# Performance work log

Measured on AMD Instinct MI355X. Metric: run time of the kernel, lower is better.

Reference implementation:

```python
import jax, jax.numpy as jnp
import numpy as np

IMG = 160      # img_size
P = 100        # img_pathch_num = (160/16)^2
NBLK = 256     # pixels per 16x16 patch
NCLS = 4

def _index_matrix():
    # faithful port of NewAIFV.index_init
    ind = np.arange(256)
    start = (ind // 16) * IMG + (ind % 16) * 16
    idx = np.zeros(NBLK * P, dtype=np.int32)
    for i in range(P):
        idx[i * 256:(i + 1) * 256] = start + (i // 16) * 16 * IMG + (i % 16)
    return jnp.asarray(idx)

_IDX = _index_matrix()


def setup_inputs() -> dict:
    key = jax.random.key(0)
    ks = jax.random.split(key, 7)
    B, C = 4, 256
    return {
        "feat_S": jax.random.normal(ks[0], (B, C, IMG, IMG), jnp.float32),
        "feat_T": jax.random.normal(ks[1], (B, C, IMG, IMG), jnp.float32),
        "Pred_S": jax.random.normal(ks[2], (B, NCLS, IMG, IMG), jnp.float32),
        "Pred_T": jax.random.normal(ks[3], (B, NCLS, IMG, IMG), jnp.float32),
        "S_atten": jax.random.normal(ks[4], (B, P, P), jnp.float32),
        "T_atten": jax.random.normal(ks[5], (B, P, P), jnp.float32),
        "target": jax.random.randint(ks[6], (B, 1, IMG, IMG), 0, NCLS, jnp.int32),
    }


def _cos(a, b):
    # torch.nn.CosineSimilarity(dim=1): dot / max(|a||b|, 1e-8)
    num = (a * b).sum(1)
    den = jnp.maximum(jnp.sqrt((a * a).sum(1)) * jnp.sqrt((b * b).sum(1)), 1e-8)
    return num / den


def reference(feat_S, feat_T, Pred_S, Pred_T, S_atten, T_atten, target):
    B, C, H, W = feat_S.shape
    hw = H * W
    idx = _IDX
    # gathered patch reorder (index_select along flattened spatial dim)
    fS = feat_S.reshape(B, C, hw)[:, :, idx]
    fT = feat_T.reshape(B, C, hw)[:, :, idx]
    tg = target.reshape(B, 1, hw)[:, :, idx].reshape(B, 1, H, W)
    # 256-iteration loop of per-patch [B,C,100]@[B,100,100] matmuls -> one einsum
    TS = jnp.einsum('bcik,bkj->bcij', fS.reshape(B, C, NBLK, P), S_atten).reshape(B, C, H, W)
    TT = jnp.einsum('bcik,bkj->bcij', fT.reshape(B, C, NBLK, P), T_atten).reshape(B, C, H, W)
    ScS = jax.nn.softmax(Pred_S, axis=1).reshape(B, NCLS, hw)[:, :, idx].reshape(B, NCLS, H, W)
    ScT = jax.nn.softmax(Pred_T, axis=1).reshape(B, NCLS, hw)[:, :, idx].reshape(B, NCLS, H, W)
    dt = TS.dtype
    one_hot = (tg == jnp.arange(NCLS)[None, :, None, None]).astype(dt)   # [B,4,H,W]
    wei_s = (ScS * one_hot).sum(1)  # [B,H,W]
    wei_t = (ScT * one_hot).sum(1)
    tf = tg.astype(dt)  # [B,1,H,W], broadcast replaces nn.Upsample+expand

    def centers(class_list, s_prto, t_prto, eps):
        cS, cT = TS, TT
        for i in range(NCLS):
            j = class_list[i]
            stmp = ScT[:, j:j + 1]              # [B,1,H,W] (Score_Tmp, broadcast over C)
            m = (tf == i).astype(dt)            # mask_feat (class i)
            mp = (tf == j).astype(dt)           # mask_feat_prto (class class_list[i])
            denS = (mp if s_prto else m).sum((-1, -2)) + eps          # [B,1]
            protoS = ((mp * TS).sum((-1, -2)) / denS)[:, :, None, None]
            denT = (stmp * (mp if t_prto else m)).sum((-1, -2)) + eps
            protoT = ((mp * TT * stmp).sum((-1, -2)) / denT)[:, :, None, None]
            cS = (1 - m) * cS + m * protoS
            cT = (1 - m) * cT + m * protoT
        return cS, cT

    # three variants exactly as in the torch loops (denominator choices differ)
    cS0, cT0 = centers([1, 0, 3, 2], False, False, 1e-6)
    cS1, cT1 = centers([2, 3, 0, 1], True, True, 1e-6)
    cS2, cT2 = centers([3, 2, 1, 0], True, True, 1.0)

    w = (1 - wei_s) * wei_t
    vec_s = jnp.stack([w * _cos(TS, c) for c in (cS0, cS1, cS2)], axis=1)  # [B,3,H,W]
    vec_t = jnp.stack([w * _cos(TT, c) for c in (cT0, cT1, cT2)], axis=1)
    return jnp.mean((vec_s - vec_t) ** 2)
```

## Files before the change

kernel.cpp:

```cpp
#include <hip/hip_runtime.h>
#include <cstdint>
#include <cstddef>

#define HW 25600

typedef __attribute__((ext_vector_type(8))) short bf16x8;
typedef __attribute__((ext_vector_type(16))) float f32x16;

union ABu { bf16x8 v; uint2 u[2]; };

__device__ __forceinline__ f32x16 zero16() {
    f32x16 z;
#pragma unroll
    for (int i = 0; i < 16; ++i) z[i] = 0.f;
    return z;
}

__device__ __forceinline__ unsigned short f2bf(float x) {
    unsigned u = __builtin_bit_cast(unsigned, x);
    unsigned r = (u + 0x7FFF + ((u >> 16) & 1)) >> 16;
    return (unsigned short)r;
}

__device__ __forceinline__ float bf2f(unsigned short s) {
    return __builtin_bit_cast(float, (unsigned)s << 16);
}

__device__ __forceinline__ float wred(float v) {
#pragma unroll
    for (int off = 32; off; off >>= 1) v += __shfl_down(v, off, 64);
    return v;
}

__device__ double blockReduce256D(double v, double* s4) {
#pragma unroll
    for (int off = 32; off; off >>= 1) v += __shfl_down(v, off, 64);
    __syncthreads();
    if ((threadIdx.x & 63) == 0) s4[threadIdx.x >> 6] = v;
    __syncthreads();
    return s4[0] + s4[1] + s4[2] + s4[3];
}

__global__ __launch_bounds__(256) void k1_prep(
    const float* __restrict__ PredS, const float* __restrict__ PredT,
    const int* __restrict__ target,
    int* __restrict__ cls_arr, float* __restrict__ wT_arr,
    float* __restrict__ w_arr, float* __restrict__ partial_prep)
{
    __shared__ float sL[4][20];
    int blk = blockIdx.x;
    int b = blk / 100, r = blk - b * 100;
    int t = threadIdx.x, w = t >> 6, lane = t & 63;
    int ql = r * 256 + t;
    int v = ((t >> 4) * 160) + ((t & 15) * 16) + ((r >> 4) * 2560) + (r & 15);

    int cls = target[b * HW + v];

    const float* pS = PredS + b * 4 * HW + v;
    float a0 = pS[0], a1 = pS[HW], a2 = pS[2 * HW], a3 = pS[3 * HW];
    float mS = fmaxf(fmaxf(a0, a1), fmaxf(a2, a3));
    float e0 = expf(a0 - mS), e1 = expf(a1 - mS), e2 = expf(a2 - mS), e3 = expf(a3 - mS);
    float invS = 1.0f / (e0 + e1 + e2 + e3);
    float wei_s = ((cls == 0) ? e0 : (cls == 1) ? e1 : (cls == 2) ? e2 : e3) * invS;

    const float* pT = PredT + b * 4 * HW + v;
    float c0 = pT[0], c1 = pT[HW], c2 = pT[2 * HW], c3 = pT[3 * HW];
    float mT = fmaxf(fmaxf(c0, c1), fmaxf(c2, c3));
    float f0 = expf(c0 - mT), f1 = expf(c1 - mT), f2 = expf(c2 - mT), f3 = expf(c3 - mT);
    float invT = 1.0f / (f0 + f1 + f2 + f3);
    float tn0 = f0 * invT, tn1 = f1 * invT, tn2 = f2 * invT, tn3 = f3 * invT;
    float wei_t = (cls == 0) ? tn0 : (cls == 1) ? tn1 : (cls == 2) ? tn2 : tn3;

    cls_arr[b * HW + ql] = cls;
    wT_arr[b * HW + ql] = wei_t;
    w_arr[b * HW + ql] = (1.0f - wei_s) * wei_t;

    float vals[20];
#pragma unroll
    for (int s = 0; s < 4; ++s) vals[s] = (cls == s) ? 1.f : 0.f;
#pragma unroll
    for (int i2 = 0; i2 < 4; ++i2) {
        vals[4 + i2 * 4 + 0] = (cls == i2) ? tn0 : 0.f;
        vals[4 + i2 * 4 + 1] = (cls == i2) ? tn1 : 0.f;
        vals[4 + i2 * 4 + 2] = (cls == i2) ? tn2 : 0.f;
        vals[4 + i2 * 4 + 3] = (cls == i2) ? tn3 : 0.f;
    }
#pragma unroll
    for (int s = 0; s < 20; ++s) {
        float rv = wred(vals[s]);
        if (lane == 0) sL[w][s] = rv;
    }
    __syncthreads();
    if (t < 20) {
        int ob = blk * 20;
        partial_prep[ob + t] = sL[0][t] + sL[1][t] + sL[2][t] + sL[3][t];
    }
}

__global__ void k15_red(const float* __restrict__ partial_prep,
                        float* __restrict__ cnt, float* __restrict__ E)
{
    int t = threadIdx.x;
    if (t < 80) {
        int b = t / 20, s = t - (t / 20) * 20;
        float a = 0.f;
        for (int r = 0; r < 100; ++r) a += partial_prep[(b * 100 + r) * 20 + s];
        if (s < 4) cnt[b * 4 + s] = a;
        else       E[b * 16 + (s - 4)] = a;
    }
}

__global__ __launch_bounds__(128) void k2_w(
    const float* __restrict__ Satt, const float* __restrict__ Tatt,
    const int* __restrict__ cls_arr, const float* __restrict__ wT_arr,
    unsigned short* __restrict__ Wbf_S, unsigned short* __restrict__ Wbf_T)
{
    __shared__ float Al[100 * 101];
    __shared__ int cls_s[100];
    __shared__ float wTs[100];
    int blk = blockIdx.x;
    int b = blk >> 8, i = blk & 255;
    int t = threadIdx.x;
    if (t < 100) {
        cls_s[t] = cls_arr[b * HW + i * 100 + t];
        wTs[t] = wT_arr[b * HW + i * 100 + t];
    }
    for (int f = t; f < 10000; f += 128) Al[f + f / 100] = Satt[b * 10000 + f];
    __syncthreads();
    if (t < 100) {
        float a0 = 0, a1 = 0, a2 = 0, a3 = 0;
        for (int jc = 0; jc < 100; ++jc) {
            float a = Al[t * 101 + jc];
            int cc = cls_s[jc];
            a0 += (cc == 0) ? a : 0.f;
            a1 += (cc == 1) ? a : 0.f;
            a2 += (cc == 2) ? a : 0.f;
            a3 += (cc == 3) ? a : 0.f;
        }
        uint2 pk;
        pk.x = (unsigned)f2bf(a0) | ((unsigned)f2bf(a1) << 16);
        pk.y = (unsigned)f2bf(a2) | ((unsigned)f2bf(a3) << 16);
        *(uint2*)(Wbf_S + (size_t)(b * HW + i * 100 + t) * 4) = pk;
    }
    __syncthreads();
    for (int f = t; f < 10000; f += 128) Al[f + f / 100] = Tatt[b * 10000 + f];
    __syncthreads();
    if (t < 100) {
        float a0 = 0, a1 = 0, a2 = 0, a3 = 0;
        for (int jc = 0; jc < 100; ++jc) {
            float a = Al[t * 101 + jc] * wTs[jc];
            int cc = cls_s[jc];
            a0 += (cc == 0) ? a : 0.f;
            a1 += (cc == 1) ? a : 0.f;
            a2 += (cc == 2) ? a : 0.f;
            a3 += (cc == 3) ? a : 0.f;
        }
        uint2 pk;
        pk.x = (unsigned)f2bf(a0) | ((unsigned)f2bf(a1) << 16);
        pk.y = (unsigned)f2bf(a2) | ((unsigned)f2bf(a3) << 16);
        *(uint2*)(Wbf_T + (size_t)(b * HW + i * 100 + t) * 4) = pk;
    }
}

__global__ __launch_bounds__(256) void k3_scan(
    const float* __restrict__ feat, const unsigned short* __restrict__ Wbf,
    unsigned short* __restrict__ featP, float* __restrict__ pp)
{
    __shared__ unsigned short ldsW[16 * 260 + 8];
    __shared__ float sL[16];
    int x = blockIdx.x;
    int c = x & 255;
    int bd = x >> 8;
    int D = bd % 7, b = bd / 7;
    int t = threadIdx.x, w = t >> 6, lane = t & 63;

    const float* fbase = feat + (size_t)(b * 256 + c) * HW + 2560 * D;
#pragma unroll
    for (int ra = 0; ra < 4; ++ra) {
        int A = (t >> 6) + 4 * ra;
        int f4i = t & 63;
        float4 fx = *(const float4*)(fbase + 160 * A + 4 * f4i);
        uint2 pk;
        pk.x = (unsigned)f2bf(fx.x) | ((unsigned)f2bf(fx.y) << 16);
        pk.y = (unsigned)f2bf(fx.z) | ((unsigned)f2bf(fx.w) << 16);
        *(uint2*)(ldsW + A * 260 + 4 * f4i) = pk;
    }
    __syncthreads();

    float as0 = 0.f, as1 = 0.f, as2 = 0.f, as3 = 0.f;
    int nr = (D < 6) ? 2 : 1;
    for (int rep = 0; rep < nr; ++rep) {
        if (D == 6 && t >= 128) break;
        int pl = rep * 2048 + t * 8;
        int Pb = D * 4096 + pl;
        int4 w4[4];
        {
            const int4* wp = (const int4*)(Wbf + ((size_t)b * HW + Pb) * 4);
            w4[0] = wp[0]; w4[1] = wp[1]; w4[2] = wp[2]; w4[3] = wp[3];
        }
        int A = (t & 31) >> 1;
        int base_unit = A * 260 + 128 * (t & 1) + rep * 8 + (t >> 5);
        unsigned short us[8];
        float fv[8];
#pragma unroll
        for (int e = 0; e < 8; ++e) {
            us[e] = ldsW[base_unit + 16 * e];
            fv[e] = bf2f(us[e]);
        }
        const unsigned short* ww = (const unsigned short*)w4;
#pragma unroll
        for (int e = 0; e < 8; ++e) {
            as0 += fv[e] * bf2f(ww[e * 4 + 0]);
            as1 += fv[e] * bf2f(ww[e * 4 + 1]);
            as2 += fv[e] * bf2f(ww[e * 4 + 2]);
            as3 += fv[e] * bf2f(ww[e * 4 + 3]);
        }
        int4 outp;
        ((unsigned*)&outp)[0] = (unsigned)us[0] | ((unsigned)us[1] << 16);
        ((unsigned*)&outp)[1] = (unsigned)us[2] | ((unsigned)us[3] << 16);
        ((unsigned*)&outp)[2] = (unsigned)us[4] | ((unsigned)us[5] << 16);
        ((unsigned*)&outp)[3] = (unsigned)us[6] | ((unsigned)us[7] << 16);
        *(int4*)(featP + (size_t)(b * 256 + c) * HW + Pb) = outp;
    }

    float rv0 = wred(as0), rv1 = wred(as1), rv2 = wred(as2), rv3 = wred(as3);
    if (lane == 0) {
        sL[w * 4 + 0] = rv0; sL[w * 4 + 1] = rv1;
        sL[w * 4 + 2] = rv2; sL[w * 4 + 3] = rv3;
    }
    __syncthreads();
    if (t < 4) {
        pp[x * 4 + t] = sL[t] + sL[4 + t] + sL[8 + t] + sL[12 + t];
    }
}

__global__ void k35_red(const float* __restrict__ pp, float* __restrict__ Sum)
{
    int id = blockIdx.x * 256 + threadIdx.x;
    if (id < 4096) {
        int bc = id >> 2, j = id & 3;
        int b = bc >> 8, c = bc & 255;
        float a = 0.f;
        for (int D = 0; D < 7; ++D)
            a += pp[(((b * 7 + D) * 256) + c) * 4 + j];
        Sum[id] = a;
    }
}

__global__ __launch_bounds__(256, 2) void k4_mfma(
    const unsigned short* __restrict__ featP,
    const float* __restrict__ Att,
    const float* __restrict__ Sum,
    float* __restrict__ n2h, float* __restrict__ doth)
{
    __shared__ __align__(16) unsigned short featL[32 * 408 + 16];
    __shared__ __align__(16) unsigned short attL[100 * 136];

    int x = blockIdx.x;
    int chalf = x & 1, b = (x >> 1) & 3, g = x >> 3;
    int t = threadIdx.x, w = t >> 6, l = t & 63;

    for (int f = t; f < 13600; f += 256) attL[f] = 0;
    featL[(t >> 3) * 408 + 400 + (t & 7)] = 0;
    if (t < 16) featL[32 * 408 + t] = 0;
    __syncthreads();
    for (int f = t; f < 10000; f += 256) {
        int k = f / 100, j = f - k * 100;
        attL[j * 136 + k] = f2bf(Att[b * 10000 + f]);
    }

    float n2a[4] = {0, 0, 0, 0};
    float dota[4][4] = {};

    int lj = l & 31, lh = l >> 5;
    const unsigned short* brow0 = attL + (0 * 32 + lj) * 136 + lh * 8;
    const unsigned short* brow1 = attL + (1 * 32 + lj) * 136 + lh * 8;
    const unsigned short* brow2 = attL + (2 * 32 + lj) * 136 + lh * 8;
    int j3 = 96 + lj; if (j3 > 99) j3 = 99;
    const unsigned short* brow3 = attL + j3 * 136 + lh * 8;
    const unsigned short* arow = featL + lj * 408 + w * 100 + lh * 8;

#pragma unroll 1
    for (int ch = 0; ch < 4; ++ch) {
        __syncthreads();
        {
            const unsigned short* src = featP + (size_t)(b * 256 + chalf * 128 + ch * 32 + (t >> 3)) * HW
                                        + g * 400 + (t & 7) * 8;
            unsigned short* dst = featL + (t >> 3) * 408 + (t & 7) * 8;
#pragma unroll
            for (int i = 0; i < 7; ++i) {
                int cb = (t & 7) + i * 8;
                if (cb < 50)
                    *(int4*)(dst + i * 64) = *(const int4*)(src + i * 64);
            }
        }
        __syncthreads();

        f32x16 acc0 = zero16(), acc1 = zero16(), acc2 = zero16(), acc3 = zero16();
#pragma unroll
        for (int ks = 0; ks < 7; ++ks) {
            ABu aF;
            aF.u[0] = *(const uint2*)(arow + ks * 16);
            aF.u[1] = *(const uint2*)(arow + ks * 16 + 4);
            bf16x8 b0 = *(const bf16x8*)(brow0 + ks * 16);
            acc0 = __builtin_amdgcn_mfma_f32_32x32x16_bf16(aF.v, b0, acc0, 0, 0, 0);
            bf16x8 b1 = *(const bf16x8*)(brow1 + ks * 16);
            acc1 = __builtin_amdgcn_mfma_f32_32x32x16_bf16(aF.v, b1, acc1, 0, 0, 0);
            bf16x8 b2 = *(const bf16x8*)(brow2 + ks * 16);
            acc2 = __builtin_amdgcn_mfma_f32_32x32x16_bf16(aF.v, b2, acc2, 0, 0, 0);
            bf16x8 b3 = *(const bf16x8*)(brow3 + ks * 16);
            acc3 = __builtin_amdgcn_mfma_f32_32x32x16_bf16(aF.v, b3, acc3, 0, 0, 0);
        }

        int cb0 = chalf * 128 + ch * 32 + (lh << 2);
#pragma unroll
        for (int r = 0; r < 16; ++r) {
            int cl = (r & 3) + ((r >> 2) << 3);
            float4 sv = *(const float4*)(Sum + (size_t)(b * 256 + cb0 + cl) * 4);
            float v;
            v = acc0[r]; n2a[0] += v * v;
            dota[0][0] += v * sv.x; dota[0][1] += v * sv.y; dota[0][2] += v * sv.z; dota[0][3] += v * sv.w;
            v = acc1[r]; n2a[1] += v * v;
            dota[1][0] += v * sv.x; dota[1][1] += v * sv.y; dota[1][2] += v * sv.z; dota[1][3] += v * sv.w;
            v = acc2[r]; n2a[2] += v * v;
            dota[2][0] += v * sv.x; dota[2][1] += v * sv.y; dota[2][2] += v * sv.z; dota[2][3] += v * sv.w;
            v = acc3[r]; n2a[3] += v * v;
            dota[3][0] += v * sv.x; dota[3][1] += v * sv.y; dota[3][2] += v * sv.z; dota[3][3] += v * sv.w;
        }
    }

#pragma unroll
    for (int nt = 0; nt < 4; ++nt) {
        n2a[nt] += __shfl_down(n2a[nt], 32, 64);
#pragma unroll
        for (int m = 0; m < 4; ++m) dota[nt][m] += __shfl_down(dota[nt][m], 32, 64);
    }
    if (l < 32) {
        int i0 = g * 4 + w;
        int pqb = b * HW + i0 * 100;
#pragma unroll
        for (int nt = 0; nt < 4; ++nt) {
            int j = nt * 32 + l;
            if (j < 100) {
                n2h[chalf * 102400 + pqb + j] = n2a[nt];
                float4 dv = {dota[nt][0], dota[nt][1], dota[nt][2], dota[nt][3]};
                *(float4*)(doth + chalf * 409600 + (size_t)(pqb + j) * 4) = dv;
            }
        }
    }
}

__global__ void k45_tbl(const float* __restrict__ SumTS, const float* __restrict__ SumTT,
                        const float* __restrict__ cnt, const float* __restrict__ E,
                        float* __restrict__ tbl)
{
    int t = threadIdx.x;
    if (t < 32) {
        int b = t >> 3, sj = t & 7, stv = sj >> 2, j = sj & 3;
        const float* S = stv ? SumTT : SumTS;
        float s = 0.f;
        for (int c = 0; c < 256; ++c) {
            float x = S[(b * 256 + c) * 4 + j];
            s += x * x;
        }
        tbl[b * 32 + stv * 4 + j] = sqrtf(s);
    } else if (t < 48) {
        int q = t - 32;
        int b = q >> 2, i = q & 3;
        tbl[b * 32 + 8 + 0 * 4 + i] = cnt[b * 4 + i] + 1e-6f;
        tbl[b * 32 + 8 + 1 * 4 + i] = cnt[b * 4 + (i ^ 2)] + 1e-6f;
        tbl[b * 32 + 8 + 2 * 4 + i] = cnt[b * 4 + (i ^ 3)] + 1.0f;
        tbl[b * 32 + 20 + 0 * 4 + i] = E[b * 16 + i * 4 + (i ^ 1)] + 1e-6f;
        tbl[b * 32 + 20 + 1 * 4 + i] = E[b * 16 + 5 * (i ^ 2)] + 1e-6f;
        tbl[b * 32 + 20 + 2 * 4 + i] = E[b * 16 + 5 * (i ^ 3)] + 1.0f;
    }
}

__global__ __launch_bounds__(256) void k5_final(
    const int* __restrict__ cls_arr, const float* __restrict__ w_arr,
    const float* __restrict__ n2S, const float* __restrict__ n2T,
    const float* __restrict__ dotS, const float* __restrict__ dotT,
    const float* __restrict__ tbl, double* __restrict__ partial_res)
{
    __shared__ double s4[4];
    int blk = blockIdx.x;
    int b = blk / 100, r = blk - b * 100;
    int t = threadIdx.x;
    int pq = b * HW + r * 256 + t;

    int i = cls_arr[pq];
    float wv = w_arr[pq];
    float sqS = sqrtf(n2S[pq] + n2S[102400 + pq]);
    float sqT = sqrtf(n2T[pq] + n2T[102400 + pq]);
    float4 dSa = *(const float4*)(dotS + (size_t)pq * 4);
    float4 dSb = *(const float4*)(dotS + 409600 + (size_t)pq * 4);
    float4 dTa = *(const float4*)(dotT + (size_t)pq * 4);
    float4 dTb = *(const float4*)(dotT + 409600 + (size_t)pq * 4);
    float4 dS = {dSa.x + dSb.x, dSa.y + dSb.y, dSa.z + dSb.z, dSa.w + dSb.w};
    float4 dT = {dTa.x + dTb.x, dTa.y + dTb.y, dTa.z + dTb.z, dTa.w + dTb.w};
    const float* tb = tbl + b * 32;

    double acc = 0.0;
#pragma unroll
    for (int v = 0; v < 3; ++v) {
        int j = i ^ (v + 1);
        float dsj = (j == 0) ? dS.x : (j == 1) ? dS.y : (j == 2) ? dS.z : dS.w;
        float dtj = (j == 0) ? dT.x : (j == 1) ? dT.y : (j == 2) ? dT.z : dT.w;
        float cnS = tb[j], cnT = tb[4 + j];
        float denS = tb[8 + v * 4 + i], denT = tb[20 + v * 4 + i];
        float cs = (dsj / denS) / fmaxf(sqS * (cnS / denS), 1e-8f);
        float ct = (dtj / denT) / fmaxf(sqT * (cnT / denT), 1e-8f);
        float vs = wv * cs, vt = wv * ct;
        float d = vs - vt;
        acc += (double)d * (double)d;
    }
    double tot = blockReduce256D(acc, s4);
    if (t == 0) partial_res[blk] = tot;
}

__global__ void k6_out(const double* __restrict__ partial_res, float* __restrict__ out)
{
    if (threadIdx.x == 0 && blockIdx.x == 0) {
        double s = 0.0;
        for (int q = 0; q < 400; ++q) s += partial_res[q];
        out[0] = (float)(s / 307200.0);
    }
}

extern "C" void kernel_launch(void* const* d_in, const int* in_sizes, int n_in,
                              void* d_out, int out_size, void* d_ws, size_t ws_size,
                              hipStream_t stream)
{
    const float* feat_S  = (const float*)d_in[0];
    const float* feat_T  = (const float*)d_in[1];
    const float* Pred_S  = (const float*)d_in[2];
    const float* Pred_T  = (const float*)d_in[3];
    const float* S_atten = (const float*)d_in[4];
    const float* T_atten = (const float*)d_in[5];
    const int*   target  = (const int*)d_in[6];

    float* ws = (float*)d_ws;
    unsigned short* featP = (unsigned short*)d_ws;
    unsigned short* WbfS  = (unsigned short*)(ws + 13107200);
    unsigned short* WbfT  = (unsigned short*)(ws + 13312000);
    int*   cls_a = (int*)(ws + 13516800);
    float* wT_a  = ws + 13619200;
    float* w_a   = ws + 13721600;
    float* SumTS = ws + 13824000;
    float* SumTT = ws + 13828096;
    float* n2S   = ws + 13832192;
    float* n2T   = ws + 14036992;
    float* dotS  = ws + 14241792;
    float* dotT  = ws + 15060992;
    float* pprep = ws + 15880192;
    float* cnt   = ws + 15888192;
    float* E     = ws + 15888208;
    float* tbl   = ws + 15888272;
    double* pres = (double*)(ws + 15888400);
    float* ppart = ws + 15889200;

    k1_prep<<<400, 256, 0, stream>>>(Pred_S, Pred_T, target, cls_a, wT_a, w_a, pprep);
    k15_red<<<1, 128, 0, stream>>>(pprep, cnt, E);
    k2_w<<<1024, 128, 0, stream>>>(S_atten, T_atten, cls_a, wT_a, WbfS, WbfT);

    k3_scan<<<7168, 256, 0, stream>>>(feat_S, WbfS, featP, ppart);
    k35_red<<<16, 256, 0, stream>>>(ppart, SumTS);
    k4_mfma<<<512, 256, 0, stream>>>(featP, S_atten, SumTS, n2S, dotS);
    k3_scan<<<7168, 256, 0, stream>>>(feat_T, WbfT, featP, ppart);
    k35_red<<<16, 256, 0, stream>>>(ppart, SumTT);
    k4_mfma<<<512, 256, 0, stream>>>(featP, T_atten, SumTT, n2T, dotT);

    k45_tbl<<<1, 64, 0, stream>>>(SumTS, SumTT, cnt, E, tbl);
    k5_final<<<400, 256, 0, stream>>>(cls_a, w_a, n2S, n2T, dotS, dotT, tbl, pres);
    k6_out<<<1, 64, 0, stream>>>(pres, (float*)d_out);
}
```

Baseline: 173.2 us.

## Merge S/T passes into single launches and parallelize small reductions

Processes the student and teacher sides in the same k3_scan and k4_mfma launches by doubling the grid and giving each side its own featP buffer. k3_scan now handles four channels per block and reuses the attention weights kept in registers across them. k4_mfma preloads the B operand into registers instead of reading it from LDS on every step. The k15 reduction is folded into k2_w as extra blocks, and k45_tbl and k6_out become wave and block reductions rather than serial loops. This cuts the launch count and exposes more parallelism, at the cost of a workspace twice as large and more register pressure in k4.

```diff
diff --git a/kernel.cpp b/kernel.cpp
--- a/kernel.cpp
+++ b/kernel.cpp
@@ -8,6 +8,7 @@
 typedef __attribute__((ext_vector_type(16))) float f32x16;
 
 union ABu { bf16x8 v; uint2 u[2]; };
+union B128 { bf16x8 v; int4 q; };
 
 __device__ __forceinline__ f32x16 zero16() {
     f32x16 z;
@@ -97,30 +98,29 @@
     }
 }
 
-__global__ void k15_red(const float* __restrict__ partial_prep,
-                        float* __restrict__ cnt, float* __restrict__ E)
-{
-    int t = threadIdx.x;
-    if (t < 80) {
-        int b = t / 20, s = t - (t / 20) * 20;
-        float a = 0.f;
-        for (int r = 0; r < 100; ++r) a += partial_prep[(b * 100 + r) * 20 + s];
-        if (s < 4) cnt[b * 4 + s] = a;
-        else       E[b * 16 + (s - 4)] = a;
-    }
-}
-
 __global__ __launch_bounds__(128) void k2_w(
     const float* __restrict__ Satt, const float* __restrict__ Tatt,
     const int* __restrict__ cls_arr, const float* __restrict__ wT_arr,
-    unsigned short* __restrict__ Wbf_S, unsigned short* __restrict__ Wbf_T)
-{
+    unsigned short* __restrict__ Wbf_S, unsigned short* __restrict__ Wbf_T,
+    const float* __restrict__ partial_prep, float* __restrict__ cnt, float* __restrict__ E)
+{
+    int blk = blockIdx.x;
+    int t = threadIdx.x;
+    if (blk >= 1024) {
+        int i = blk - 1024;
+        if (t < 64) {
+            int b = i / 20, s = i - (i / 20) * 20;
+            float a = partial_prep[(b * 100 + t) * 20 + s];
+            if (t + 64 < 100) a += partial_prep[(b * 100 + t + 64) * 20 + s];
+            a = wred(a);
+            if (t == 0) { if (s < 4) cnt[b * 4 + s] = a; else E[b * 16 + (s - 4)] = a; }
+        }
+        return;
+    }
     __shared__ float Al[100 * 101];
     __shared__ int cls_s[100];
     __shared__ float wTs[100];
-    int blk = blockIdx.x;
     int b = blk >> 8, i = blk & 255;
-    int t = threadIdx.x;
     if (t < 100) {
         cls_s[t] = cls_arr[b * HW + i * 100 + t];
         wTs[t] = wT_arr[b * HW + i * 100 + t];
@@ -163,102 +163,129 @@
 }
 
 __global__ __launch_bounds__(256) void k3_scan(
-    const float* __restrict__ feat, const unsigned short* __restrict__ Wbf,
+    const float* __restrict__ featS, const float* __restrict__ featT,
+    const unsigned short* __restrict__ WbfS, const unsigned short* __restrict__ WbfT,
     unsigned short* __restrict__ featP, float* __restrict__ pp)
 {
     __shared__ unsigned short ldsW[16 * 260 + 8];
     __shared__ float sL[16];
     int x = blockIdx.x;
-    int c = x & 255;
-    int bd = x >> 8;
+    int side = x & 1;
+    int rest = x >> 1;
+    int cq = rest & 63;
+    int bd = rest >> 6;
     int D = bd % 7, b = bd / 7;
     int t = threadIdx.x, w = t >> 6, lane = t & 63;
 
-    const float* fbase = feat + (size_t)(b * 256 + c) * HW + 2560 * D;
-#pragma unroll
-    for (int ra = 0; ra < 4; ++ra) {
-        int A = (t >> 6) + 4 * ra;
-        int f4i = t & 63;
-        float4 fx = *(const float4*)(fbase + 160 * A + 4 * f4i);
-        uint2 pk;
-        pk.x = (unsigned)f2bf(fx.x) | ((unsigned)f2bf(fx.y) << 16);
-        pk.y = (unsigned)f2bf(fx.z) | ((unsigned)f2bf(fx.w) << 16);
-        *(uint2*)(ldsW + A * 260 + 4 * f4i) = pk;
-    }
-    __syncthreads();
-
-    float as0 = 0.f, as1 = 0.f, as2 = 0.f, as3 = 0.f;
+    const float* feat = side ? featT : featS;
+    const unsigned short* Wbf = side ? WbfT : WbfS;
+    unsigned short* fP = featP + (size_t)side * 26214400u;
+    int ppbase = side * 28672 + ((b * 7 + D) * 256) * 4;
+
     int nr = (D < 6) ? 2 : 1;
-    for (int rep = 0; rep < nr; ++rep) {
-        if (D == 6 && t >= 128) break;
-        int pl = rep * 2048 + t * 8;
-        int Pb = D * 4096 + pl;
-        int4 w4[4];
-        {
+    bool act = !(D == 6 && t >= 128);
+
+    int4 w4[2][4];
+#pragma unroll
+    for (int rep = 0; rep < 2; ++rep) {
+        if (rep < nr && act) {
+            int Pb = D * 4096 + rep * 2048 + t * 8;
             const int4* wp = (const int4*)(Wbf + ((size_t)b * HW + Pb) * 4);
-            w4[0] = wp[0]; w4[1] = wp[1]; w4[2] = wp[2]; w4[3] = wp[3];
-        }
-        int A = (t & 31) >> 1;
-        int base_unit = A * 260 + 128 * (t & 1) + rep * 8 + (t >> 5);
-        unsigned short us[8];
-        float fv[8];
-#pragma unroll
-        for (int e = 0; e < 8; ++e) {
-            us[e] = ldsW[base_unit + 16 * e];
-            fv[e] = bf2f(us[e]);
-        }
-        const unsigned short* ww = (const unsigned short*)w4;
-#pragma unroll
-        for (int e = 0; e < 8; ++e) {
-            as0 += fv[e] * bf2f(ww[e * 4 + 0]);
-            as1 += fv[e] * bf2f(ww[e * 4 + 1]);
-            as2 += fv[e] * bf2f(ww[e * 4 + 2]);
-            as3 += fv[e] * bf2f(ww[e * 4 + 3]);
-        }
-        int4 outp;
-        ((unsigned*)&outp)[0] = (unsigned)us[0] | ((unsigned)us[1] << 16);
-        ((unsigned*)&outp)[1] = (unsigned)us[2] | ((unsigned)us[3] << 16);
-        ((unsigned*)&outp)[2] = (unsigned)us[4] | ((unsigned)us[5] << 16);
-        ((unsigned*)&outp)[3] = (unsigned)us[6] | ((unsigned)us[7] << 16);
-        *(int4*)(featP + (size_t)(b * 256 + c) * HW + Pb) = outp;
-    }
-
-    float rv0 = wred(as0), rv1 = wred(as1), rv2 = wred(as2), rv3 = wred(as3);
-    if (lane == 0) {
-        sL[w * 4 + 0] = rv0; sL[w * 4 + 1] = rv1;
-        sL[w * 4 + 2] = rv2; sL[w * 4 + 3] = rv3;
-    }
-    __syncthreads();
-    if (t < 4) {
-        pp[x * 4 + t] = sL[t] + sL[4 + t] + sL[8 + t] + sL[12 + t];
-    }
-}
-
-__global__ void k35_red(const float* __restrict__ pp, float* __restrict__ Sum)
+            w4[rep][0] = wp[0]; w4[rep][1] = wp[1]; w4[rep][2] = wp[2]; w4[rep][3] = wp[3];
+        }
+    }
+
+    for (int cv = 0; cv < 4; ++cv) {
+        int c = cq * 4 + cv;
+        const float* fbase = feat + (size_t)(b * 256 + c) * HW + 2560 * D;
+#pragma unroll
+        for (int ra = 0; ra < 4; ++ra) {
+            int A = (t >> 6) + 4 * ra;
+            int f4i = t & 63;
+            float4 fx = *(const float4*)(fbase + 160 * A + 4 * f4i);
+            uint2 pk;
+            pk.x = (unsigned)f2bf(fx.x) | ((unsigned)f2bf(fx.y) << 16);
+            pk.y = (unsigned)f2bf(fx.z) | ((unsigned)f2bf(fx.w) << 16);
+            *(uint2*)(ldsW + A * 260 + 4 * f4i) = pk;
+        }
+        __syncthreads();
+
+        float as0 = 0.f, as1 = 0.f, as2 = 0.f, as3 = 0.f;
+        if (act) {
+#pragma unroll
+            for (int rep = 0; rep < 2; ++rep) {
+                if (rep < nr) {
+                    int Pb = D * 4096 + rep * 2048 + t * 8;
+                    int A2 = (t & 31) >> 1;
+                    int base_unit = A2 * 260 + 128 * (t & 1) + rep * 8 + (t >> 5);
+                    unsigned short us[8];
+                    float fv[8];
+#pragma unroll
+                    for (int e = 0; e < 8; ++e) {
+                        us[e] = ldsW[base_unit + 16 * e];
+                        fv[e] = bf2f(us[e]);
+                    }
+                    const unsigned short* ww = (const unsigned short*)w4[rep];
+#pragma unroll
+                    for (int e = 0; e < 8; ++e) {
+                        as0 += fv[e] * bf2f(ww[e * 4 + 0]);
+                        as1 += fv[e] * bf2f(ww[e * 4 + 1]);
+                        as2 += fv[e] * bf2f(ww[e * 4 + 2]);
+                        as3 += fv[e] * bf2f(ww[e * 4 + 3]);
+                    }
+                    int4 outp;
+                    ((unsigned*)&outp)[0] = (unsigned)us[0] | ((unsigned)us[1] << 16);
+                    ((unsigned*)&outp)[1] = (unsigned)us[2] | ((unsigned)us[3] << 16);
+                    ((unsigned*)&outp)[2] = (unsigned)us[4] | ((unsigned)us[5] << 16);
+                    ((unsigned*)&outp)[3] = (unsigned)us[6] | ((unsigned)us[7] << 16);
+                    *(int4*)(fP + (size_t)(b * 256 + c) * HW + Pb) = outp;
+                }
+            }
+        }
+
+        float rv0 = wred(as0), rv1 = wred(as1), rv2 = wred(as2), rv3 = wred(as3);
+        if (lane == 0) {
+            sL[w * 4 + 0] = rv0; sL[w * 4 + 1] = rv1;
+            sL[w * 4 + 2] = rv2; sL[w * 4 + 3] = rv3;
+        }
+        __syncthreads();
+        if (t < 4) pp[ppbase + c * 4 + t] = sL[t] + sL[4 + t] + sL[8 + t] + sL[12 + t];
+        __syncthreads();
+    }
+}
+
+__global__ void k35_red(const float* __restrict__ pp, float* __restrict__ SumAll)
 {
     int id = blockIdx.x * 256 + threadIdx.x;
-    if (id < 4096) {
-        int bc = id >> 2, j = id & 3;
-        int b = bc >> 8, c = bc & 255;
-        float a = 0.f;
-        for (int D = 0; D < 7; ++D)
-            a += pp[(((b * 7 + D) * 256) + c) * 4 + j];
-        Sum[id] = a;
-    }
+    int side = id >> 12;
+    int rem = id & 4095;
+    int bc = rem >> 2, j = rem & 3;
+    int b = bc >> 8, c = bc & 255;
+    float a = 0.f;
+    for (int D = 0; D < 7; ++D)
+        a += pp[side * 28672 + (((b * 7 + D) * 256) + c) * 4 + j];
+    SumAll[side * 4096 + bc * 4 + j] = a;
 }
 
 __global__ __launch_bounds__(256, 2) void k4_mfma(
     const unsigned short* __restrict__ featP,
-    const float* __restrict__ Att,
-    const float* __restrict__ Sum,
-    float* __restrict__ n2h, float* __restrict__ doth)
+    const float* __restrict__ SattG, const float* __restrict__ TattG,
+    const float* __restrict__ SumAll,
+    float* __restrict__ n2S, float* __restrict__ n2T,
+    float* __restrict__ dotS, float* __restrict__ dotT)
 {
     __shared__ __align__(16) unsigned short featL[32 * 408 + 16];
     __shared__ __align__(16) unsigned short attL[100 * 136];
 
     int x = blockIdx.x;
-    int chalf = x & 1, b = (x >> 1) & 3, g = x >> 3;
+    int side = x & 1, chalf = (x >> 1) & 1, b = (x >> 2) & 3, g = x >> 4;
     int t = threadIdx.x, w = t >> 6, l = t & 63;
+
+    const float* Att = side ? TattG : SattG;
+    const float* Sum = SumAll + side * 4096;
+    const unsigned short* fP = featP + (size_t)side * 26214400u;
+    float* n2h = side ? n2T : n2S;
+    float* doth = side ? dotT : dotS;
 
     for (int f = t; f < 13600; f += 256) attL[f] = 0;
     featL[(t >> 3) * 408 + 400 + (t & 7)] = 0;
@@ -268,23 +295,29 @@
         int k = f / 100, j = f - k * 100;
         attL[j * 136 + k] = f2bf(Att[b * 10000 + f]);
     }
+    __syncthreads();
+
+    int lj = l & 31, lh = l >> 5;
+    bf16x8 breg[7][4];
+    {
+        int j3 = 96 + lj; if (j3 > 99) j3 = 99;
+        int rowoff[4] = { lj, 32 + lj, 64 + lj, j3 };
+#pragma unroll
+        for (int ks = 0; ks < 7; ++ks)
+#pragma unroll
+            for (int s = 0; s < 4; ++s)
+                breg[ks][s] = ((const B128*)(attL + rowoff[s] * 136 + lh * 8 + ks * 16))->v;
+    }
 
     float n2a[4] = {0, 0, 0, 0};
     float dota[4][4] = {};
-
-    int lj = l & 31, lh = l >> 5;
-    const unsigned short* brow0 = attL + (0 * 32 + lj) * 136 + lh * 8;
-    const unsigned short* brow1 = attL + (1 * 32 + lj) * 136 + lh * 8;
-    const unsigned short* brow2 = attL + (2 * 32 + lj) * 136 + lh * 8;
-    int j3 = 96 + lj; if (j3 > 99) j3 = 99;
-    const unsigned short* brow3 = attL + j3 * 136 + lh * 8;
     const unsigned short* arow = featL + lj * 408 + w * 100 + lh * 8;
 
 #pragma unroll 1
     for (int ch = 0; ch < 4; ++ch) {
         __syncthreads();
         {
-            const unsigned short* src = featP + (size_t)(b * 256 + chalf * 128 + ch * 32 + (t >> 3)) * HW
+            const unsigned short* src = fP + (size_t)(b * 256 + chalf * 128 + ch * 32 + (t >> 3)) * HW
                                         + g * 400 + (t & 7) * 8;
             unsigned short* dst = featL + (t >> 3) * 408 + (t & 7) * 8;
 #pragma unroll
@@ -302,14 +335,10 @@
             ABu aF;
             aF.u[0] = *(const uint2*)(arow + ks * 16);
             aF.u[1] = *(const uint2*)(arow + ks * 16 + 4);
-            bf16x8 b0 = *(const bf16x8*)(brow0 + ks * 16);
-            acc0 = __builtin_amdgcn_mfma_f32_32x32x16_bf16(aF.v, b0, acc0, 0, 0, 0);
-            bf16x8 b1 = *(const bf16x8*)(brow1 + ks * 16);
-            acc1 = __builtin_amdgcn_mfma_f32_32x32x16_bf16(aF.v, b1, acc1, 0, 0, 0);
-            bf16x8 b2 = *(const bf16x8*)(brow2 + ks * 16);
-            acc2 = __builtin_amdgcn_mfma_f32_32x32x16_bf16(aF.v, b2, acc2, 0, 0, 0);
-            bf16x8 b3 = *(const bf16x8*)(brow3 + ks * 16);
-            acc3 = __builtin_amdgcn_mfma_f32_32x32x16_bf16(aF.v, b3, acc3, 0, 0, 0);
+            acc0 = __builtin_amdgcn_mfma_f32_32x32x16_bf16(aF.v, breg[ks][0], acc0, 0, 0, 0);
+            acc1 = __builtin_amdgcn_mfma_f32_32x32x16_bf16(aF.v, breg[ks][1], acc1, 0, 0, 0);
+            acc2 = __builtin_amdgcn_mfma_f32_32x32x16_bf16(aF.v, breg[ks][2], acc2, 0, 0, 0);
+            acc3 = __builtin_amdgcn_mfma_f32_32x32x16_bf16(aF.v, breg[ks][3], acc3, 0, 0, 0);
         }
 
         int cb0 = chalf * 128 + ch * 32 + (lh << 2);
@@ -354,19 +383,20 @@
                         const float* __restrict__ cnt, const float* __restrict__ E,
                         float* __restrict__ tbl)
 {
-    int t = threadIdx.x;
-    if (t < 32) {
-        int b = t >> 3, sj = t & 7, stv = sj >> 2, j = sj & 3;
+    int blk = blockIdx.x, t = threadIdx.x;
+    if (blk < 32) {
+        int b = blk >> 3, sj = blk & 7, stv = sj >> 2, j = sj & 3;
         const float* S = stv ? SumTT : SumTS;
         float s = 0.f;
-        for (int c = 0; c < 256; ++c) {
-            float x = S[(b * 256 + c) * 4 + j];
-            s += x * x;
-        }
-        tbl[b * 32 + stv * 4 + j] = sqrtf(s);
-    } else if (t < 48) {
-        int q = t - 32;
-        int b = q >> 2, i = q & 3;
+#pragma unroll
+        for (int u = 0; u < 4; ++u) {
+            float xx = S[(b * 256 + t * 4 + u) * 4 + j];
+            s += xx * xx;
+        }
+        s = wred(s);
+        if (t == 0) tbl[b * 32 + stv * 4 + j] = sqrtf(s);
+    } else if (t < 16) {
+        int b = t >> 2, i = t & 3;
         tbl[b * 32 + 8 + 0 * 4 + i] = cnt[b * 4 + i] + 1e-6f;
         tbl[b * 32 + 8 + 1 * 4 + i] = cnt[b * 4 + (i ^ 2)] + 1e-6f;
         tbl[b * 32 + 8 + 2 * 4 + i] = cnt[b * 4 + (i ^ 3)] + 1.0f;
@@ -418,13 +448,14 @@
     if (t == 0) partial_res[blk] = tot;
 }
 
-__global__ void k6_out(const double* __restrict__ partial_res, float* __restrict__ out)
-{
-    if (threadIdx.x == 0 && blockIdx.x == 0) {
-        double s = 0.0;
-        for (int q = 0; q < 400; ++q) s += partial_res[q];
-        out[0] = (float)(s / 307200.0);
-    }
+__global__ __launch_bounds__(256) void k6_out(const double* __restrict__ partial_res,
+                                              float* __restrict__ out)
+{
+    __shared__ double s4[4];
+    int t = threadIdx.x;
+    double v = (t < 200) ? (partial_res[t] + partial_res[t + 200]) : 0.0;
+    double tot = blockReduce256D(v, s4);
+    if (t == 0) out[0] = (float)(tot / 307200.0);
 }
 
 extern "C" void kernel_launch(void* const* d_in, const int* in_sizes, int n_in,
@@ -441,36 +472,30 @@
 
     float* ws = (float*)d_ws;
     unsigned short* featP = (unsigned short*)d_ws;
-    unsigned short* WbfS  = (unsigned short*)(ws + 13107200);
-    unsigned short* WbfT  = (unsigned short*)(ws + 13312000);
-    int*   cls_a = (int*)(ws + 13516800);
-    float* wT_a  = ws + 13619200;
-    float* w_a   = ws + 13721600;
-    float* SumTS = ws + 13824000;
-    float* SumTT = ws + 13828096;
-    float* n2S   = ws + 13832192;
-    float* n2T   = ws + 14036992;
-    float* dotS  = ws + 14241792;
-    float* dotT  = ws + 15060992;
-    float* pprep = ws + 15880192;
-    float* cnt   = ws + 15888192;
-    float* E     = ws + 15888208;
-    float* tbl   = ws + 15888272;
-    double* pres = (double*)(ws + 15888400);
-    float* ppart = ws + 15889200;
+    unsigned short* WbfS  = (unsigned short*)(ws + 26214400);
+    unsigned short* WbfT  = (unsigned short*)(ws + 26419200);
+    int*   cls_a = (int*)(ws + 26624000);
+    float* wT_a  = ws + 26726400;
+    float* w_a   = ws + 26828800;
+    float* SumTS = ws + 26931200;
+    float* SumTT = ws + 26935296;
+    float* n2S   = ws + 26939392;
+    float* n2T   = ws + 27144192;
+    float* dotS  = ws + 27348992;
+    float* dotT  = ws + 28168192;
+    float* pprep = ws + 28987392;
+    float* cnt   = ws + 28995392;
+    float* E     = ws + 28995408;
+    float* tbl   = ws + 28995472;
+    double* pres = (double*)(ws + 28995600);
+    float* ppart = ws + 28996400;
 
     k1_prep<<<400, 256, 0, stream>>>(Pred_S, Pred_T, target, cls_a, wT_a, w_a, pprep);
-    k15_red<<<1, 128, 0, stream>>>(pprep, cnt, E);
-    k2_w<<<1024, 128, 0, stream>>>(S_atten, T_atten, cls_a, wT_a, WbfS, WbfT);
-
-    k3_scan<<<7168, 256, 0, stream>>>(feat_S, WbfS, featP, ppart);
-    k35_red<<<16, 256, 0, stream>>>(ppart, SumTS);
-    k4_mfma<<<512, 256, 0, stream>>>(featP, S_atten, SumTS, n2S, dotS);
-    k3_scan<<<7168, 256, 0, stream>>>(feat_T, WbfT, featP, ppart);
-    k35_red<<<16, 256, 0, stream>>>(ppart, SumTT);
-    k4_mfma<<<512, 256, 0, stream>>>(featP, T_atten, SumTT, n2T, dotT);
-
-    k45_tbl<<<1, 64, 0, stream>>>(SumTS, SumTT, cnt, E, tbl);
+    k2_w<<<1104, 128, 0, stream>>>(S_atten, T_atten, cls_a, wT_a, WbfS, WbfT, pprep, cnt, E);
+    k3_scan<<<3584, 256, 0, stream>>>(feat_S, feat_T, WbfS, WbfT, featP, ppart);
+    k35_red<<<32, 256, 0, stream>>>(ppart, SumTS);
+    k4_mfma<<<1024, 256, 0, stream>>>(featP, S_atten, T_atten, SumTS, n2S, n2T, dotS, dotT);
+    k45_tbl<<<33, 64, 0, stream>>>(SumTS, SumTT, cnt, E, tbl);
     k5_final<<<400, 256, 0, stream>>>(cls_a, w_a, n2S, n2T, dotS, dotT, tbl, pres);
-    k6_out<<<1, 64, 0, stream>>>(pres, (float*)d_out);
-}
+    k6_out<<<1, 256, 0, stream>>>(pres, (float*)d_out);
+}
```

Result: faster. 155.0 us (-10.5%).
